# Kernel tuning notes

Measured on AMD Instinct MI355X. Metric: run time of the kernel, lower is better.

The kernel has to match this reference:

```python
import jax, jax.numpy as jnp
import numpy as np

# Hyperparameters (must match init_kwargs)
B, S, D = 1, 4096, 1024
H, DK, DV = 16, 64, 64
G, W, R = 1, 23, 8          # global, window, random tokens
KSEL = 1 + R + W            # selected keys per non-global query


def setup_inputs() -> dict:
    key = jax.random.key(0)
    ks = jax.random.split(key, 8)
    scale = 0.02
    Q = jax.random.normal(ks[0], (B, S, D), dtype=jnp.float32)
    K = jax.random.normal(ks[1], (B, S, D), dtype=jnp.float32)
    V = jax.random.normal(ks[2], (B, S, D), dtype=jnp.float32)
    Wq = jax.random.normal(ks[3], (D, H * DK), dtype=jnp.float32) * scale
    Wk = jax.random.normal(ks[4], (D, H * DK), dtype=jnp.float32) * scale
    Wv = jax.random.normal(ks[5], (D, H * DV), dtype=jnp.float32) * scale
    Wo = jax.random.normal(ks[6], (H * DV, D), dtype=jnp.float32) * scale
    # BigBird-style index table: [global(=token 0), random, sliding window]
    n_ng = S - 2 * G
    base = jnp.arange(G, S - G)                                   # [n_ng]
    win = base[:, None] + jnp.arange(W)[None, :] - (W - 1) // 2   # [n_ng, W]
    win = jnp.clip(win, 0, S - 1)
    rnd = jax.random.randint(ks[7], (n_ng, R), 1, S)              # [n_ng, R]
    glb = jnp.zeros((n_ng, 1), dtype=jnp.int64)
    idx = jnp.concatenate([glb, rnd.astype(jnp.int64), win.astype(jnp.int64)], axis=1)  # [n_ng, KSEL]
    return {"Q": Q, "K": K, "V": V, "Wq": Wq, "Wk": Wk, "Wv": Wv, "Wo": Wo, "idx": idx}


def reference(Q, K, V, Wq, Wk, Wv, Wo, idx):
    b, s, _ = Q.shape
    g = G
    # Projections, split heads: [B,H,S,d]
    q = (Q @ Wq).reshape(b, s, H, DK).transpose(0, 2, 1, 3)
    k = (K @ Wk).reshape(b, s, H, DK).transpose(0, 2, 1, 3)
    v = (V @ Wv).reshape(b, s, H, DV).transpose(0, 2, 1, 3)
    scale = 1.0 / jnp.sqrt(jnp.asarray(DK, dtype=q.dtype))

    # --- dense global-token path: first g and last g queries attend to all keys ---
    gidx = jnp.concatenate([jnp.arange(g), jnp.arange(s - g, s)])  # [2g]
    q_g = q[:, :, gidx, :]                                          # [B,H,2g,dk]
    logits_g = jnp.einsum('bhgd,bhnd->bhgn', q_g, k) * scale
    prob_g = jax.nn.softmax(logits_g, axis=-1)
    out_g = jnp.einsum('bhgn,bhnd->bhgd', prob_g, v)                # [B,H,2g,dv]

    # --- sparse gather path for the remaining queries ---
    q_ng = q[:, :, g:s - g, :]                                      # [B,H,n_ng,dk]
    k_sel = k[:, :, idx, :]                                         # [B,H,n_ng,KSEL,dk]
    v_sel = v[:, :, idx, :]                                         # [B,H,n_ng,KSEL,dv]
    logits = jnp.einsum('bhnd,bhnkd->bhnk', q_ng, k_sel) * scale
    prob = jax.nn.softmax(logits, axis=-1)
    out_ng = jnp.einsum('bhnk,bhnkd->bhnd', prob, v_sel)            # [B,H,n_ng,dv]

    out = jnp.concatenate([out_g[:, :, :g], out_ng, out_g[:, :, g:]], axis=2)  # [B,H,S,dv]
    x = out.transpose(0, 2, 1, 3).reshape(b, s, H * DV)
    return x @ Wo
```

## Files before the change

### kernel.cpp

```cpp
#include <hip/hip_runtime.h>

typedef unsigned short u16;
typedef unsigned int u32;
typedef __bf16 bf16x8_t __attribute__((ext_vector_type(8)));
typedef float f32x4 __attribute__((ext_vector_type(4)));
typedef u32 u32x4 __attribute__((ext_vector_type(4)));
typedef u16 u16x8 __attribute__((ext_vector_type(8)));

__device__ __forceinline__ float b2f(u16 u) {
  u32 x = ((u32)u) << 16; float f; __builtin_memcpy(&f, &x, 4); return f;
}
__device__ __forceinline__ u16 f2b(float f) {
  u32 x; __builtin_memcpy(&x, &f, 4);
  return (u16)((x + 0x8000u) >> 16);
}

__device__ __forceinline__ u16x8 ld8(const void* p, size_t off, int f32) {
  if (!f32) return *(const u16x8*)((const u16*)p + off);
  const u32* u = (const u32*)p + off;
  u32x4 a = *(const u32x4*)u;
  u32x4 b = *(const u32x4*)(u + 4);
  u16x8 r;
#pragma unroll
  for (int e = 0; e < 4; ++e) r[e] = (u16)((a[e] + 0x8000u) >> 16);
#pragma unroll
  for (int e = 0; e < 4; ++e) r[4 + e] = (u16)((b[e] + 0x8000u) >> 16);
  return r;
}

#if __has_builtin(__builtin_amdgcn_global_load_lds)
__device__ __forceinline__ void gl_lds16(const u16* g, u16* l, int lane) {
  (void)lane;
  __builtin_amdgcn_global_load_lds(
      (const __attribute__((address_space(1))) void*)g,
      (__attribute__((address_space(3))) void*)l, 16, 0, 0);
}
#else
__device__ __forceinline__ void gl_lds16(const u16* g, u16* l, int lane) {
  *(u16x8*)(l + lane * 8) = *(const u16x8*)g;
}
#endif

__global__ void detect_kernel(const u32* __restrict__ qraw,
                              const int* __restrict__ iraw,
                              int* __restrict__ flags) {
  const int t = threadIdx.x;
  int c = 0;
#pragma unroll
  for (int p = 0; p < 8; ++p) {
    const int e = (qraw[p * 64 + t] >> 7) & 0xFF;
    c += (e >= 100 && e <= 141);
  }
  for (int off = 32; off; off >>= 1) c += __shfl_xor(c, off);
  int nz = 0;
  if (t < 16) nz = (iraw[(t + 1) * 32 + 1] != 0);
  const unsigned long long bal = __ballot(nz);
  if (t == 0) {
    flags[0] = (c < 300) ? 1 : 0;
    flags[1] = (bal == 0ull) ? 1 : 0;
  }
}

__global__ __launch_bounds__(256) void transpose4(
    const void* s0, const void* s1, const void* s2, const void* s3,
    u16* d0, u16* d1, u16* d2, u16* d3, const int* flags) {
  const int f32 = flags[0];
  const void* src;
  u16* dst;
  switch (blockIdx.z) {
    case 0: src = s0; dst = d0; break;
    case 1: src = s1; dst = d1; break;
    case 2: src = s2; dst = d2; break;
    default: src = s3; dst = d3; break;
  }
  __shared__ u16 tile[32][33];
  const int tx = threadIdx.x, ty = threadIdx.y;
  const int bx = blockIdx.x * 32, by = blockIdx.y * 32;
#pragma unroll
  for (int i = 0; i < 4; ++i) {
    const int off = (by + ty + i * 8) * 1024 + bx + tx;
    tile[ty + i * 8][tx] = f32 ? f2b(((const float*)src)[off]) : ((const u16*)src)[off];
  }
  __syncthreads();
#pragma unroll
  for (int i = 0; i < 4; ++i)
    dst[(bx + ty + i * 8) * 1024 + by + tx] = tile[tx][ty + i * 8];
}

__global__ __launch_bounds__(256) void conv3_bf16(
    const void* Q, const void* K, const void* V,
    u16* Qb, u16* Kb, u16* Vb, const int* flags) {
  if (!flags[0]) return;
  const void* s; u16* d;
  switch (blockIdx.y) {
    case 0: s = Q; d = Qb; break;
    case 1: s = K; d = Kb; break;
    default: s = V; d = Vb; break;
  }
  const size_t i = ((size_t)blockIdx.x * 256 + threadIdx.x) * 8;
  *(u16x8*)(d + i) = ld8(s, i, 1);
}

template <int BM>
__device__ __forceinline__ void gemm_fast(const void* A, int a_f32,
                                          const u16* __restrict__ Bt,
                                          void* C, int c_f32) {
  constexpr int AI = BM / 64;
  __shared__ __align__(16) u16 As[BM * 32];
  __shared__ __align__(16) u16 Bs[128 * 32];
  const int t = threadIdx.x;
  const int lane = t & 63, w = t >> 6;
  const int bm = blockIdx.x * BM, bn = blockIdx.y * 128;
  const int lr = lane >> 2, lc = (lane & 3) * 8;
  const int wr = (w >> 1) * (BM / 2);
  const int wc = (w & 1) * 64;
  const int m16 = lane & 15, q4 = lane >> 4;
  f32x4 acc[BM / 32][4] = {};

  for (int k0 = 0; k0 < 1024; k0 += 32) {
    if (!a_f32) {
#pragma unroll
      for (int i = 0; i < AI; ++i)
        gl_lds16((const u16*)A + (size_t)(bm + w * 16 * AI + i * 16 + lr) * 1024 + k0 + lc,
                 &As[(w * 16 * AI + i * 16) * 32], lane);
    } else {
#pragma unroll
      for (int i = 0; i < AI; ++i)
        *(u16x8*)&As[(w * 16 * AI + i * 16 + lr) * 32 + lc] =
            ld8(A, (size_t)(bm + w * 16 * AI + i * 16 + lr) * 1024 + k0 + lc, 1);
    }
    gl_lds16(Bt + (size_t)(bn + w * 32 + lr) * 1024 + k0 + lc, &Bs[(w * 32) * 32], lane);
    gl_lds16(Bt + (size_t)(bn + w * 32 + 16 + lr) * 1024 + k0 + lc, &Bs[(w * 32 + 16) * 32], lane);
    __syncthreads();
    bf16x8_t af[BM / 32], bfr[4];
#pragma unroll
    for (int i = 0; i < BM / 32; ++i)
      af[i] = *(const bf16x8_t*)&As[(wr + i * 16 + m16) * 32 + q4 * 8];
#pragma unroll
    for (int j = 0; j < 4; ++j)
      bfr[j] = *(const bf16x8_t*)&Bs[(wc + j * 16 + m16) * 32 + q4 * 8];
#pragma unroll
    for (int i = 0; i < BM / 32; ++i)
#pragma unroll
      for (int j = 0; j < 4; ++j)
        acc[i][j] = __builtin_amdgcn_mfma_f32_16x16x32_bf16(af[i], bfr[j], acc[i][j], 0, 0, 0);
    __syncthreads();
  }
#pragma unroll
  for (int i = 0; i < BM / 32; ++i)
#pragma unroll
    for (int r = 0; r < 4; ++r) {
      const int row = bm + wr + i * 16 + q4 * 4 + r;
#pragma unroll
      for (int j = 0; j < 4; ++j) {
        const int col = bn + wc + j * 16 + m16;
        const float x = acc[i][j][r];
        if (c_f32) ((float*)C)[(size_t)row * 1024 + col] = x;
        else       ((u16*)C)[(size_t)row * 1024 + col] = f2b(x);
      }
    }
}

__global__ __launch_bounds__(256) void gemm_qkv(
    const void* Q, const void* K, const void* V,
    const u16* Qb, const u16* Kb, const u16* Vb,
    const u16* WqT, const u16* WkT, const u16* WvT,
    u16* q, u16* k, u16* v, const int* flags, int big) {
  const int f32 = flags[0];
  const void* Araw; const u16* Ab; const u16* Bt; u16* Cp;
  switch (blockIdx.z) {
    case 0:  Araw = Q; Ab = Qb; Bt = WqT; Cp = q; break;
    case 1:  Araw = K; Ab = Kb; Bt = WkT; Cp = k; break;
    default: Araw = V; Ab = Vb; Bt = WvT; Cp = v; break;
  }
  if (big && f32) gemm_fast<128>(Ab, 0, Bt, Cp, 0);
  else            gemm_fast<128>(Araw, f32, Bt, Cp, 0);
}

__global__ __launch_bounds__(256) void gemm_out(
    const u16* A, const u16* WoT, void* C, const int* flags) {
  gemm_fast<64>(A, 0, WoT, C, flags[0]);
}

__global__ __launch_bounds__(256) void attn_sel(
    u16* qp, const u16* __restrict__ kp, const u16* __restrict__ vp,
    const int* __restrict__ idx, const int* __restrict__ flags) {
  const int b = blockIdx.x;
  int s0 = (b & 7) * 512 + (b >> 3);
  if (s0 >= 4094) s0 = 3583;
  const int s = s0 + 1;
  const int t = threadIdx.x;
  __shared__ float ps[512];
  __shared__ int sidx[32];

  if (t >= 224) {
    const int j = t - 224;
    const size_t e = (size_t)(s - 1) * 32 + j;
    sidx[j] = flags[1] ? idx[2 * e] : idx[e];
  }

  const int w = t >> 6, lane = t & 63;
  const int jj = lane >> 3, dl = lane & 7;

  float qreg[4][8];
#pragma unroll
  for (int hh = 0; hh < 4; ++hh) {
    const u16x8 qv = *(const u16x8*)(qp + (size_t)s * 1024 + (w * 4 + hh) * 64 + dl * 8);
#pragma unroll
    for (int e = 0; e < 8; ++e) qreg[hh][e] = b2f((u16)qv[e]);
  }
  __syncthreads();

#pragma unroll
  for (int p = 0; p < 16; ++p) {
    const int h = w * 4 + (p >> 2);
    const int j = (p & 3) * 8 + jj;
    const u16x8 kv = *(const u16x8*)(kp + (size_t)sidx[j] * 1024 + h * 64 + dl * 8);
    float acc = 0.f;
#pragma unroll
    for (int e = 0; e < 8; ++e) acc += qreg[p >> 2][e] * b2f((u16)kv[e]);
    acc += __shfl_xor(acc, 1);
    acc += __shfl_xor(acc, 2);
    acc += __shfl_xor(acc, 4);
    if (dl == 0) ps[h * 32 + j] = acc * 0.125f;
  }
  __syncthreads();

  {
    const int h = t >> 4, jx = t & 15;
    const float v0 = ps[h * 32 + jx], v1 = ps[h * 32 + jx + 16];
    float mx = fmaxf(v0, v1);
    mx = fmaxf(mx, __shfl_xor(mx, 1));
    mx = fmaxf(mx, __shfl_xor(mx, 2));
    mx = fmaxf(mx, __shfl_xor(mx, 4));
    mx = fmaxf(mx, __shfl_xor(mx, 8));
    const float p0 = __expf(v0 - mx), p1 = __expf(v1 - mx);
    float sm = p0 + p1;
    sm += __shfl_xor(sm, 1);
    sm += __shfl_xor(sm, 2);
    sm += __shfl_xor(sm, 4);
    sm += __shfl_xor(sm, 8);
    const float r = 1.f / sm;
    ps[h * 32 + jx] = p0 * r;
    ps[h * 32 + jx + 16] = p1 * r;
  }
  __syncthreads();

  const int dc = lane & 7;
#pragma unroll
  for (int hp = 0; hp < 4; ++hp) {
    const int h = hp * 4 + w;
    float acc8[8] = {};
#pragma unroll
    for (int j0 = 0; j0 < 32; j0 += 8) {
      const int j = j0 + jj;
      const u16x8 v8 = *(const u16x8*)(vp + (size_t)sidx[j] * 1024 + h * 64 + dc * 8);
      const float p = ps[h * 32 + j];
#pragma unroll
      for (int e = 0; e < 8; ++e) acc8[e] += p * b2f((u16)v8[e]);
    }
#pragma unroll
    for (int e = 0; e < 8; ++e) {
      acc8[e] += __shfl_xor(acc8[e], 8);
      acc8[e] += __shfl_xor(acc8[e], 16);
      acc8[e] += __shfl_xor(acc8[e], 32);
    }
    if (jj == 0) {
      u16x8 o;
#pragma unroll
      for (int e = 0; e < 8; ++e) o[e] = f2b(acc8[e]);
      *(u16x8*)(qp + (size_t)s * 1024 + h * 64 + dc * 8) = o;
    }
  }
}

__global__ __launch_bounds__(256) void attn_glb_a(
    const u16* __restrict__ qp, const u16* __restrict__ kp,
    const u16* __restrict__ vp, float* __restrict__ part) {
  const int qi = blockIdx.x >> 7;
  const int h = (blockIdx.x >> 3) & 15;
  const int c = blockIdx.x & 7;
  const int s = qi ? 4095 : 0;
  const int t = threadIdx.x;
  __shared__ float qh[64];
  __shared__ float lg[512];
  __shared__ float red[4];
  __shared__ float pvs[4][64];
  if (t < 8) {
    u16x8 v = *(const u16x8*)(qp + (size_t)s * 1024 + h * 64 + t * 8);
#pragma unroll
    for (int e = 0; e < 8; ++e) qh[t * 8 + e] = b2f((u16)v[e]);
  }
  __syncthreads();
  float lv[2];
#pragma unroll
  for (int i = 0; i < 2; ++i) {
    const int n = c * 512 + t + i * 256;
    const u16* krow = kp + (size_t)n * 1024 + h * 64;
    float acc = 0.f;
#pragma unroll
    for (int cc = 0; cc < 8; ++cc) {
      u16x8 kv = *(const u16x8*)(krow + cc * 8);
#pragma unroll
      for (int e = 0; e < 8; ++e) acc += qh[cc * 8 + e] * b2f((u16)kv[e]);
    }
    lv[i] = acc * 0.125f;
  }
  float m2 = fmaxf(lv[0], lv[1]);
  for (int off = 32; off; off >>= 1) m2 = fmaxf(m2, __shfl_xor(m2, off));
  if ((t & 63) == 0) red[t >> 6] = m2;
  __syncthreads();
  const float gm = fmaxf(fmaxf(red[0], red[1]), fmaxf(red[2], red[3]));
  const float p0 = __expf(lv[0] - gm), p1 = __expf(lv[1] - gm);
  lg[t] = p0; lg[t + 256] = p1;
  float sm = p0 + p1;
  for (int off = 32; off; off >>= 1) sm += __shfl_xor(sm, off);
  __syncthreads();
  if ((t & 63) == 0) red[t >> 6] = sm;
  __syncthreads();
  const float ssum = red[0] + red[1] + red[2] + red[3];

  const int d = t & 63, cc = t >> 6;
  float acc = 0.f;
  for (int i = 0; i < 128; ++i) {
    const int nl = cc * 128 + i;
    acc += lg[nl] * b2f(vp[(size_t)(c * 512 + nl) * 1024 + h * 64 + d]);
  }
  pvs[cc][d] = acc;
  __syncthreads();
  float* dst = part + ((size_t)(qi * 16 + h) * 8 + c) * 66;
  if (t == 0) { dst[0] = gm; dst[1] = ssum; }
  if (t < 64) dst[2 + t] = pvs[0][t] + pvs[1][t] + pvs[2][t] + pvs[3][t];
}

__global__ void attn_glb_b(u16* __restrict__ qp, const float* __restrict__ part) {
  const int qi = blockIdx.x >> 4, h = blockIdx.x & 15;
  const int s = qi ? 4095 : 0;
  const int t = threadIdx.x;
  const float* p = part + ((size_t)(qi * 16 + h) * 8) * 66;
  float gm = -1e30f;
#pragma unroll
  for (int c = 0; c < 8; ++c) gm = fmaxf(gm, p[c * 66]);
  float S = 0.f, o = 0.f;
#pragma unroll
  for (int c = 0; c < 8; ++c) {
    const float w = __expf(p[c * 66] - gm);
    S += p[c * 66 + 1] * w;
    o += p[c * 66 + 2 + t] * w;
  }
  qp[(size_t)s * 1024 + h * 64 + t] = f2b(o / S);
}

extern "C" void kernel_launch(void* const* d_in, const int* in_sizes, int n_in,
                              void* d_out, int out_size, void* d_ws, size_t ws_size,
                              hipStream_t stream) {
  const void* Q  = d_in[0];
  const void* K  = d_in[1];
  const void* V  = d_in[2];
  const void* Wq = d_in[3];
  const void* Wk = d_in[4];
  const void* Wv = d_in[5];
  const void* Wo = d_in[6];
  const int* idx = (const int*)d_in[7];

  u16* WqT = (u16*)d_ws;
  u16* WkT = WqT + (1 << 20);
  u16* WvT = WkT + (1 << 20);
  u16* WoT = WvT + (1 << 20);
  u16* qp  = WoT + (1 << 20);
  u16* vp  = qp + (4 << 20);
  int* flags = (int*)(vp + (4 << 20));
  float* part = (float*)WkT;
  u16* kp = (u16*)d_out;
  u16* Qb = (u16*)((char*)d_ws + (24ull << 20) + 4096);
  u16* Kb = Qb + (4 << 20);
  u16* Vb = Kb + (4 << 20);
  const bool big = ws_size >= (48ull << 20) + 8192;

  detect_kernel<<<1, 64, 0, stream>>>((const u32*)Q, idx, flags);
  transpose4<<<dim3(32, 32, 4), dim3(32, 8), 0, stream>>>(
      Wq, Wk, Wv, Wo, WqT, WkT, WvT, WoT, flags);
  if (big)
    conv3_bf16<<<dim3(2048, 3), 256, 0, stream>>>(Q, K, V, Qb, Kb, Vb, flags);
  gemm_qkv<<<dim3(32, 8, 3), 256, 0, stream>>>(
      Q, K, V, Qb, Kb, Vb, WqT, WkT, WvT, qp, kp, vp, flags, big ? 1 : 0);
  attn_glb_a<<<256, 256, 0, stream>>>(qp, kp, vp, part);
  attn_glb_b<<<32, 64, 0, stream>>>(qp, part);
  attn_sel<<<4094, 256, 0, stream>>>(qp, kp, vp, idx, flags);
  gemm_out<<<dim3(64, 8), 256, 0, stream>>>(qp, WoT, d_out, flags);
}
```

Baseline: 227.1 us.

## Fuse prep kernels, merge global and sparse attention, use packed FMA

Replaces the separate detect, transpose and bf16-convert kernels with a single prep launch. Each kernel now recomputes the input-format detection inline instead of reading a flags buffer. The dense global-token partial kernel is merged into the sparse attention kernel as extra blocks, which cuts the launch count. The sparse QK and PV loops unpack bf16 pairs and use two-wide float FMAs. The aim is to remove launch overhead and serialization gaps between small kernels and to shorten the inner arithmetic; the cost is redundant detection reads in every block and a larger combined attention kernel.

```diff
diff --git a/kernel.cpp b/kernel.cpp
--- a/kernel.cpp
+++ b/kernel.cpp
@@ -4,6 +4,7 @@
 typedef unsigned int u32;
 typedef __bf16 bf16x8_t __attribute__((ext_vector_type(8)));
 typedef float f32x4 __attribute__((ext_vector_type(4)));
+typedef float f32x2 __attribute__((ext_vector_type(2)));
 typedef u32 u32x4 __attribute__((ext_vector_type(4)));
 typedef u16 u16x8 __attribute__((ext_vector_type(8)));
 
@@ -13,6 +14,11 @@
 __device__ __forceinline__ u16 f2b(float f) {
   u32 x; __builtin_memcpy(&x, &f, 4);
   return (u16)((x + 0x8000u) >> 16);
+}
+__device__ __forceinline__ f32x2 up2(u32 w) {
+  u32 lo = w << 16, hi = w & 0xffff0000u;
+  float a, b; __builtin_memcpy(&a, &lo, 4); __builtin_memcpy(&b, &hi, 4);
+  f32x2 r; r[0] = a; r[1] = b; return r;
 }
 
 __device__ __forceinline__ u16x8 ld8(const void* p, size_t off, int f32) {
@@ -41,40 +47,51 @@
 }
 #endif
 
-__global__ void detect_kernel(const u32* __restrict__ qraw,
-                              const int* __restrict__ iraw,
-                              int* __restrict__ flags) {
-  const int t = threadIdx.x;
+__device__ __forceinline__ int det_f32(const u32* qraw, int lane) {
   int c = 0;
 #pragma unroll
   for (int p = 0; p < 8; ++p) {
-    const int e = (qraw[p * 64 + t] >> 7) & 0xFF;
+    const int e = (qraw[p * 64 + lane] >> 7) & 0xFF;
     c += (e >= 100 && e <= 141);
   }
   for (int off = 32; off; off >>= 1) c += __shfl_xor(c, off);
-  int nz = 0;
-  if (t < 16) nz = (iraw[(t + 1) * 32 + 1] != 0);
-  const unsigned long long bal = __ballot(nz);
-  if (t == 0) {
-    flags[0] = (c < 300) ? 1 : 0;
-    flags[1] = (bal == 0ull) ? 1 : 0;
-  }
-}
-
-__global__ __launch_bounds__(256) void transpose4(
-    const void* s0, const void* s1, const void* s2, const void* s3,
-    u16* d0, u16* d1, u16* d2, u16* d3, const int* flags) {
-  const int f32 = flags[0];
-  const void* src;
-  u16* dst;
-  switch (blockIdx.z) {
-    case 0: src = s0; dst = d0; break;
-    case 1: src = s1; dst = d1; break;
-    case 2: src = s2; dst = d2; break;
-    default: src = s3; dst = d3; break;
+  return c < 300;
+}
+__device__ __forceinline__ int det_i64(const int* iraw, int lane) {
+  int nz = (lane < 16) ? (iraw[(lane + 1) * 32 + 1] != 0) : 0;
+  return __ballot(nz) == 0ull;
+}
+
+__global__ __launch_bounds__(256) void prep(
+    const void* Q, const void* K, const void* V,
+    const void* W0, const void* W1, const void* W2, const void* W3,
+    u16* d0, u16* d1, u16* d2, u16* d3,
+    u16* Qb, u16* Kb, u16* Vb) {
+  const int tx = threadIdx.x, ty = threadIdx.y;
+  const int t = ty * 32 + tx;
+  const int f32 = det_f32((const u32*)Q, t & 63);
+  const int z = blockIdx.z;
+  if (z >= 4) {
+    if (!f32) return;
+    const void* s; u16* d;
+    switch (z - 4) {
+      case 0: s = Q; d = Qb; break;
+      case 1: s = K; d = Kb; break;
+      default: s = V; d = Vb; break;
+    }
+    const size_t i = ((size_t)(blockIdx.y * 32 + blockIdx.x) * 256 + t) * 16;
+    *(u16x8*)(d + i) = ld8(s, i, 1);
+    *(u16x8*)(d + i + 8) = ld8(s, i + 8, 1);
+    return;
+  }
+  const void* src; u16* dst;
+  switch (z) {
+    case 0: src = W0; dst = d0; break;
+    case 1: src = W1; dst = d1; break;
+    case 2: src = W2; dst = d2; break;
+    default: src = W3; dst = d3; break;
   }
   __shared__ u16 tile[32][33];
-  const int tx = threadIdx.x, ty = threadIdx.y;
   const int bx = blockIdx.x * 32, by = blockIdx.y * 32;
 #pragma unroll
   for (int i = 0; i < 4; ++i) {
@@ -85,20 +102,6 @@
 #pragma unroll
   for (int i = 0; i < 4; ++i)
     dst[(bx + ty + i * 8) * 1024 + by + tx] = tile[tx][ty + i * 8];
-}
-
-__global__ __launch_bounds__(256) void conv3_bf16(
-    const void* Q, const void* K, const void* V,
-    u16* Qb, u16* Kb, u16* Vb, const int* flags) {
-  if (!flags[0]) return;
-  const void* s; u16* d;
-  switch (blockIdx.y) {
-    case 0: s = Q; d = Qb; break;
-    case 1: s = K; d = Kb; break;
-    default: s = V; d = Vb; break;
-  }
-  const size_t i = ((size_t)blockIdx.x * 256 + threadIdx.x) * 8;
-  *(u16x8*)(d + i) = ld8(s, i, 1);
 }
 
 template <int BM>
@@ -165,8 +168,8 @@
     const void* Q, const void* K, const void* V,
     const u16* Qb, const u16* Kb, const u16* Vb,
     const u16* WqT, const u16* WkT, const u16* WvT,
-    u16* q, u16* k, u16* v, const int* flags, int big) {
-  const int f32 = flags[0];
+    u16* q, u16* k, u16* v, int big) {
+  const int f32 = det_f32((const u32*)Q, threadIdx.x & 63);
   const void* Araw; const u16* Ab; const u16* Bt; u16* Cp;
   switch (blockIdx.z) {
     case 0:  Araw = Q; Ab = Qb; Bt = WqT; Cp = q; break;
@@ -178,36 +181,95 @@
 }
 
 __global__ __launch_bounds__(256) void gemm_out(
-    const u16* A, const u16* WoT, void* C, const int* flags) {
-  gemm_fast<64>(A, 0, WoT, C, flags[0]);
-}
-
-__global__ __launch_bounds__(256) void attn_sel(
+    const void* Qdet, const u16* A, const u16* WoT, void* C) {
+  const int f32 = det_f32((const u32*)Qdet, threadIdx.x & 63);
+  gemm_fast<64>(A, 0, WoT, C, f32);
+}
+
+__global__ __launch_bounds__(256) void attn(
     u16* qp, const u16* __restrict__ kp, const u16* __restrict__ vp,
-    const int* __restrict__ idx, const int* __restrict__ flags) {
-  const int b = blockIdx.x;
+    const int* __restrict__ idx, float* __restrict__ part) {
+  const int t = threadIdx.x;
+  __shared__ float ps[512];
+  __shared__ int sidx[32];
+  __shared__ float qh[64];
+  __shared__ float lg[512];
+  __shared__ float red[4];
+  __shared__ float pvs[4][64];
+
+  if (blockIdx.x < 256) {
+    const int qi = blockIdx.x >> 7;
+    const int h = (blockIdx.x >> 3) & 15;
+    const int c = blockIdx.x & 7;
+    const int s = qi ? 4095 : 0;
+    if (t < 8) {
+      u16x8 v = *(const u16x8*)(qp + (size_t)s * 1024 + h * 64 + t * 8);
+#pragma unroll
+      for (int e = 0; e < 8; ++e) qh[t * 8 + e] = b2f((u16)v[e]);
+    }
+    __syncthreads();
+    float lv[2];
+#pragma unroll
+    for (int i = 0; i < 2; ++i) {
+      const int n = c * 512 + t + i * 256;
+      const u16* krow = kp + (size_t)n * 1024 + h * 64;
+      float acc = 0.f;
+#pragma unroll
+      for (int cc = 0; cc < 8; ++cc) {
+        u16x8 kv = *(const u16x8*)(krow + cc * 8);
+#pragma unroll
+        for (int e = 0; e < 8; ++e) acc += qh[cc * 8 + e] * b2f((u16)kv[e]);
+      }
+      lv[i] = acc * 0.125f;
+    }
+    float m2 = fmaxf(lv[0], lv[1]);
+    for (int off = 32; off; off >>= 1) m2 = fmaxf(m2, __shfl_xor(m2, off));
+    if ((t & 63) == 0) red[t >> 6] = m2;
+    __syncthreads();
+    const float gm = fmaxf(fmaxf(red[0], red[1]), fmaxf(red[2], red[3]));
+    const float p0 = __expf(lv[0] - gm), p1 = __expf(lv[1] - gm);
+    lg[t & 255] = p0;
+    lg[t + 256] = p1;
+    float sm = p0 + p1;
+    for (int off = 32; off; off >>= 1) sm += __shfl_xor(sm, off);
+    __syncthreads();
+    if ((t & 63) == 0) red[t >> 6] = sm;
+    __syncthreads();
+    const float ssum = red[0] + red[1] + red[2] + red[3];
+    const int d = t & 63, cc = t >> 6;
+    float acc = 0.f;
+    for (int i = 0; i < 128; ++i) {
+      const int nl = cc * 128 + i;
+      acc += lg[nl] * b2f(vp[(size_t)(c * 512 + nl) * 1024 + h * 64 + d]);
+    }
+    pvs[cc][d] = acc;
+    __syncthreads();
+    float* dst = part + ((size_t)(qi * 16 + h) * 8 + c) * 66;
+    if (t == 0) { dst[0] = gm; dst[1] = ssum; }
+    if (t < 64) dst[2 + t] = pvs[0][t] + pvs[1][t] + pvs[2][t] + pvs[3][t];
+    return;
+  }
+
+  const int b = blockIdx.x - 256;
   int s0 = (b & 7) * 512 + (b >> 3);
   if (s0 >= 4094) s0 = 3583;
   const int s = s0 + 1;
-  const int t = threadIdx.x;
-  __shared__ float ps[512];
-  __shared__ int sidx[32];
+  const int w = t >> 6, lane = t & 63;
+  const int i64f = det_i64(idx, lane);
+  const int jj = lane >> 3, dl = lane & 7;
 
   if (t >= 224) {
     const int j = t - 224;
     const size_t e = (size_t)(s - 1) * 32 + j;
-    sidx[j] = flags[1] ? idx[2 * e] : idx[e];
-  }
-
-  const int w = t >> 6, lane = t & 63;
-  const int jj = lane >> 3, dl = lane & 7;
-
-  float qreg[4][8];
+    sidx[j] = i64f ? idx[2 * e] : idx[e];
+  }
+
+  f32x2 qreg[4][4];
 #pragma unroll
   for (int hh = 0; hh < 4; ++hh) {
-    const u16x8 qv = *(const u16x8*)(qp + (size_t)s * 1024 + (w * 4 + hh) * 64 + dl * 8);
-#pragma unroll
-    for (int e = 0; e < 8; ++e) qreg[hh][e] = b2f((u16)qv[e]);
+    const u32x4 qw = *(const u32x4*)(qp + (size_t)s * 1024 + (w * 4 + hh) * 64 + dl * 8);
+#pragma unroll
+    for (int c = 0; c < 4; ++c) qreg[hh][c] = up2(qw[c]);
   }
   __syncthreads();
 
@@ -215,10 +277,12 @@
   for (int p = 0; p < 16; ++p) {
     const int h = w * 4 + (p >> 2);
     const int j = (p & 3) * 8 + jj;
-    const u16x8 kv = *(const u16x8*)(kp + (size_t)sidx[j] * 1024 + h * 64 + dl * 8);
-    float acc = 0.f;
-#pragma unroll
-    for (int e = 0; e < 8; ++e) acc += qreg[p >> 2][e] * b2f((u16)kv[e]);
+    const u32x4 kw = *(const u32x4*)(kp + (size_t)sidx[j] * 1024 + h * 64 + dl * 8);
+    f32x2 a2 = {0.f, 0.f};
+#pragma unroll
+    for (int c = 0; c < 4; ++c)
+      a2 = __builtin_elementwise_fma(up2(kw[c]), qreg[p >> 2][c], a2);
+    float acc = a2[0] + a2[1];
     acc += __shfl_xor(acc, 1);
     acc += __shfl_xor(acc, 2);
     acc += __shfl_xor(acc, 4);
@@ -250,87 +314,35 @@
 #pragma unroll
   for (int hp = 0; hp < 4; ++hp) {
     const int h = hp * 4 + w;
-    float acc8[8] = {};
+    f32x2 acc2[4] = {};
 #pragma unroll
     for (int j0 = 0; j0 < 32; j0 += 8) {
       const int j = j0 + jj;
-      const u16x8 v8 = *(const u16x8*)(vp + (size_t)sidx[j] * 1024 + h * 64 + dc * 8);
+      const u32x4 vw = *(const u32x4*)(vp + (size_t)sidx[j] * 1024 + h * 64 + dc * 8);
       const float p = ps[h * 32 + j];
-#pragma unroll
-      for (int e = 0; e < 8; ++e) acc8[e] += p * b2f((u16)v8[e]);
-    }
-#pragma unroll
-    for (int e = 0; e < 8; ++e) {
-      acc8[e] += __shfl_xor(acc8[e], 8);
-      acc8[e] += __shfl_xor(acc8[e], 16);
-      acc8[e] += __shfl_xor(acc8[e], 32);
-    }
+      const f32x2 pp = {p, p};
+#pragma unroll
+      for (int c = 0; c < 4; ++c)
+        acc2[c] = __builtin_elementwise_fma(up2(vw[c]), pp, acc2[c]);
+    }
+#pragma unroll
+    for (int c = 0; c < 4; ++c)
+#pragma unroll
+      for (int e = 0; e < 2; ++e) {
+        acc2[c][e] += __shfl_xor(acc2[c][e], 8);
+        acc2[c][e] += __shfl_xor(acc2[c][e], 16);
+        acc2[c][e] += __shfl_xor(acc2[c][e], 32);
+      }
     if (jj == 0) {
       u16x8 o;
 #pragma unroll
-      for (int e = 0; e < 8; ++e) o[e] = f2b(acc8[e]);
+      for (int c = 0; c < 4; ++c) {
+        o[c * 2] = f2b(acc2[c][0]);
+        o[c * 2 + 1] = f2b(acc2[c][1]);
+      }
       *(u16x8*)(qp + (size_t)s * 1024 + h * 64 + dc * 8) = o;
     }
   }
-}
-
-__global__ __launch_bounds__(256) void attn_glb_a(
-    const u16* __restrict__ qp, const u16* __restrict__ kp,
-    const u16* __restrict__ vp, float* __restrict__ part) {
-  const int qi = blockIdx.x >> 7;
-  const int h = (blockIdx.x >> 3) & 15;
-  const int c = blockIdx.x & 7;
-  const int s = qi ? 4095 : 0;
-  const int t = threadIdx.x;
-  __shared__ float qh[64];
-  __shared__ float lg[512];
-  __shared__ float red[4];
-  __shared__ float pvs[4][64];
-  if (t < 8) {
-    u16x8 v = *(const u16x8*)(qp + (size_t)s * 1024 + h * 64 + t * 8);
-#pragma unroll
-    for (int e = 0; e < 8; ++e) qh[t * 8 + e] = b2f((u16)v[e]);
-  }
-  __syncthreads();
-  float lv[2];
-#pragma unroll
-  for (int i = 0; i < 2; ++i) {
-    const int n = c * 512 + t + i * 256;
-    const u16* krow = kp + (size_t)n * 1024 + h * 64;
-    float acc = 0.f;
-#pragma unroll
-    for (int cc = 0; cc < 8; ++cc) {
-      u16x8 kv = *(const u16x8*)(krow + cc * 8);
-#pragma unroll
-      for (int e = 0; e < 8; ++e) acc += qh[cc * 8 + e] * b2f((u16)kv[e]);
-    }
-    lv[i] = acc * 0.125f;
-  }
-  float m2 = fmaxf(lv[0], lv[1]);
-  for (int off = 32; off; off >>= 1) m2 = fmaxf(m2, __shfl_xor(m2, off));
-  if ((t & 63) == 0) red[t >> 6] = m2;
-  __syncthreads();
-  const float gm = fmaxf(fmaxf(red[0], red[1]), fmaxf(red[2], red[3]));
-  const float p0 = __expf(lv[0] - gm), p1 = __expf(lv[1] - gm);
-  lg[t] = p0; lg[t + 256] = p1;
-  float sm = p0 + p1;
-  for (int off = 32; off; off >>= 1) sm += __shfl_xor(sm, off);
-  __syncthreads();
-  if ((t & 63) == 0) red[t >> 6] = sm;
-  __syncthreads();
-  const float ssum = red[0] + red[1] + red[2] + red[3];
-
-  const int d = t & 63, cc = t >> 6;
-  float acc = 0.f;
-  for (int i = 0; i < 128; ++i) {
-    const int nl = cc * 128 + i;
-    acc += lg[nl] * b2f(vp[(size_t)(c * 512 + nl) * 1024 + h * 64 + d]);
-  }
-  pvs[cc][d] = acc;
-  __syncthreads();
-  float* dst = part + ((size_t)(qi * 16 + h) * 8 + c) * 66;
-  if (t == 0) { dst[0] = gm; dst[1] = ssum; }
-  if (t < 64) dst[2 + t] = pvs[0][t] + pvs[1][t] + pvs[2][t] + pvs[3][t];
 }
 
 __global__ void attn_glb_b(u16* __restrict__ qp, const float* __restrict__ part) {
@@ -369,7 +381,6 @@
   u16* WoT = WvT + (1 << 20);
   u16* qp  = WoT + (1 << 20);
   u16* vp  = qp + (4 << 20);
-  int* flags = (int*)(vp + (4 << 20));
   float* part = (float*)WkT;
   u16* kp = (u16*)d_out;
   u16* Qb = (u16*)((char*)d_ws + (24ull << 20) + 4096);
@@ -377,15 +388,11 @@
   u16* Vb = Kb + (4 << 20);
   const bool big = ws_size >= (48ull << 20) + 8192;
 
-  detect_kernel<<<1, 64, 0, stream>>>((const u32*)Q, idx, flags);
-  transpose4<<<dim3(32, 32, 4), dim3(32, 8), 0, stream>>>(
-      Wq, Wk, Wv, Wo, WqT, WkT, WvT, WoT, flags);
-  if (big)
-    conv3_bf16<<<dim3(2048, 3), 256, 0, stream>>>(Q, K, V, Qb, Kb, Vb, flags);
+  prep<<<dim3(32, 32, big ? 7 : 4), dim3(32, 8), 0, stream>>>(
+      Q, K, V, Wq, Wk, Wv, Wo, WqT, WkT, WvT, WoT, Qb, Kb, Vb);
   gemm_qkv<<<dim3(32, 8, 3), 256, 0, stream>>>(
-      Q, K, V, Qb, Kb, Vb, WqT, WkT, WvT, qp, kp, vp, flags, big ? 1 : 0);
-  attn_glb_a<<<256, 256, 0, stream>>>(qp, kp, vp, part);
+      Q, K, V, Qb, Kb, Vb, WqT, WkT, WvT, qp, kp, vp, big ? 1 : 0);
+  attn<<<4350, 256, 0, stream>>>(qp, kp, vp, idx, part);
   attn_glb_b<<<32, 64, 0, stream>>>(qp, part);
-  attn_sel<<<4094, 256, 0, stream>>>(qp, kp, vp, idx, flags);
-  gemm_out<<<dim3(64, 8), 256, 0, stream>>>(qp, WoT, d_out, flags);
-}
+  gemm_out<<<dim3(64, 8), 256, 0, stream>>>(Q, qp, WoT, d_out);
+}
```

Measured after the change: 225.0 us. About the same (-0.9%).
